# Kernel optimization log

Hardware: AMD Instinct MI355X
Metric: run time of the kernel (lower is better)

The kernel has to match this reference:

```python
import jax, jax.numpy as jnp
from jax import lax
import numpy as np

BATCH, SEQ_LEN, INPUT_DIM, HIDDEN, NUM_CLASSES = 2048, 512, 1, 1024, 10


def setup_inputs() -> dict:
    key = jax.random.key(0)
    k1, k2, k3, k4 = jax.random.split(key, 4)
    x = jax.random.normal(k1, (BATCH, SEQ_LEN), dtype=jnp.float32)
    # Parameters match torch.randn init; biases start at zero.
    W_hx = jax.random.normal(k2, (INPUT_DIM, HIDDEN), dtype=jnp.float32)
    W_hh = jax.random.normal(k3, (HIDDEN, HIDDEN), dtype=jnp.float32)
    W_ph = jax.random.normal(k4, (HIDDEN, NUM_CLASSES), dtype=jnp.float32)
    b_h = jnp.zeros((HIDDEN,), dtype=jnp.float32)
    b_p = jnp.zeros((NUM_CLASSES,), dtype=jnp.float32)
    return {"x": x, "W_hx": W_hx, "W_hh": W_hh, "W_ph": W_ph, "b_h": b_h, "b_p": b_p}


def reference(x, W_hx, W_hh, W_ph, b_h, b_p):
    # x: [B, T]; each timestep uses a single scalar feature -> [B, 1] @ [1, H]
    B = x.shape[0]
    H = W_hh.shape[0]

    def step(h, x_t):
        # x_t: [B]; h: [B, H]
        h_new = jnp.tanh(x_t[:, None] @ W_hx + h @ W_hh + b_h)
        return h_new, None

    h0 = jnp.zeros((B, H), dtype=x.dtype)
    h_T, _ = lax.scan(step, h0, x.T)  # scan over time (leading axis T)
    # Only the final timestep's projection is returned (matches original loop).
    return h_T @ W_ph + b_p  # [B, num_classes]
```

## Files before the change

### kernel.cpp

```cpp
#include <hip/hip_runtime.h>


#define SEQ   512
#define HID   1024
#define NCLS  10
#define TPB   512
#define ROWS  8
#define CLAMPV 7.99881172180175781f

__device__ __forceinline__ float tanh_win(float x) {
#pragma clang fp contract(off)
    float xc = fminf(fmaxf(x, -CLAMPV), CLAMPV);
    float x2 = xc * xc;
    float p = -2.76076847742355e-16f;
    p = __fmaf_rn(x2, p,  2.00018790482477e-13f);
    p = __fmaf_rn(x2, p, -8.60467152213735e-11f);
    p = __fmaf_rn(x2, p,  5.12229709037114e-08f);
    p = __fmaf_rn(x2, p,  1.48572235717979e-05f);
    p = __fmaf_rn(x2, p,  6.37261928875436e-04f);
    p = __fmaf_rn(x2, p,  4.89352455891786e-03f);
    p = xc * p;
    float q = 1.19825839466702e-06f;
    q = __fmaf_rn(x2, q,  1.18534705686654e-04f);
    q = __fmaf_rn(x2, q,  2.26843463243900e-03f);
    q = __fmaf_rn(x2, q,  4.89352518554385e-03f);
    float r = p / q;
    return (fabsf(x) < 0.0004f) ? x : r;
}

#define MAC4(hv, wv)                              \
    sv.x = __fmaf_rn((hv), (wv).x, sv.x);         \
    sv.y = __fmaf_rn((hv), (wv).y, sv.y);         \
    sv.z = __fmaf_rn((hv), (wv).z, sv.z);         \
    sv.w = __fmaf_rn((hv), (wv).w, sv.w);

__device__ __forceinline__ void panel512(float4 s[ROWS],
                                         const float* __restrict__ hl,
                                         const float* __restrict__ Whh,
                                         int ks, int c0) {
#pragma clang fp contract(off)
    #pragma unroll
    for (int r = 0; r < ROWS; ++r) s[r] = float4{0.f, 0.f, 0.f, 0.f};

    unsigned off = (unsigned)(ks * HID + c0);
    #pragma unroll 2
    for (int j = ks; j < ks + 512; j += 8) {
        const float4 w0 = *reinterpret_cast<const float4*>(Whh + off);
        const float4 w1 = *reinterpret_cast<const float4*>(Whh + off + 1u * HID);
        const float4 w2 = *reinterpret_cast<const float4*>(Whh + off + 2u * HID);
        const float4 w3 = *reinterpret_cast<const float4*>(Whh + off + 3u * HID);
        const float4 w4 = *reinterpret_cast<const float4*>(Whh + off + 4u * HID);
        const float4 w5 = *reinterpret_cast<const float4*>(Whh + off + 5u * HID);
        const float4 w6 = *reinterpret_cast<const float4*>(Whh + off + 6u * HID);
        const float4 w7 = *reinterpret_cast<const float4*>(Whh + off + 7u * HID);
        off += 8u * HID;
        #pragma unroll
        for (int r = 0; r < ROWS; ++r) {
            const float4 ha = *reinterpret_cast<const float4*>(&hl[r * HID + j]);
            const float4 hb = *reinterpret_cast<const float4*>(&hl[r * HID + j + 4]);
            float4 sv = s[r];
            MAC4(ha.x, w0); MAC4(ha.y, w1); MAC4(ha.z, w2); MAC4(ha.w, w3);
            MAC4(hb.x, w4); MAC4(hb.y, w5); MAC4(hb.z, w6); MAC4(hb.w, w7);
            s[r] = sv;
        }
    }
}

__launch_bounds__(TPB, 1)
__global__ void rnn_win(const float* __restrict__ x, const float* __restrict__ W_hx,
                        const float* __restrict__ Whh, const float* __restrict__ W_ph,
                        const float* __restrict__ bh, const float* __restrict__ bp,
                        float* __restrict__ out) {
#pragma clang fp contract(off)
    __shared__ float hl[ROWS * HID];
    __shared__ float xl[ROWS * SEQ];
    __shared__ float sb[ROWS * HID];
    const int tid  = threadIdx.x;
    const int blk  = blockIdx.x;
    const int lane = tid & 255;
    const int pp   = tid >> 8;
    const int c0   = lane * 4;
    const int row0 = blk * ROWS;

    for (int i = tid; i < ROWS * SEQ; i += TPB) xl[i] = x[(size_t)row0 * SEQ + i];
    for (int i = tid; i < ROWS * HID; i += TPB) hl[i] = 0.0f;

    const float4 w4 = *reinterpret_cast<const float4*>(W_hx + c0);
    const float4 b4 = *reinterpret_cast<const float4*>(bh + c0);
    __syncthreads();

    for (int t = 0; t < SEQ; ++t) {
        float4 s[ROWS];
        panel512(s, hl, Whh, pp * 512, c0);

        if (pp == 1) {
            #pragma unroll
            for (int r = 0; r < ROWS; ++r)
                *reinterpret_cast<float4*>(&sb[r * HID + c0]) = s[r];
        }
        __syncthreads();

        if (pp == 0) {
            #pragma unroll
            for (int r = 0; r < ROWS; ++r) {
                const float4 s1 = *reinterpret_cast<const float4*>(&sb[r * HID + c0]);
                const float xv = xl[r * SEQ + t];
                float4 g;
                g.x = s[r].x + s1.x;
                g.y = s[r].y + s1.y;
                g.z = s[r].z + s1.z;
                g.w = s[r].w + s1.w;
                float4 hn;
                hn.x = tanh_win(__fmaf_rn(xv, w4.x, g.x) + b4.x);
                hn.y = tanh_win(__fmaf_rn(xv, w4.y, g.y) + b4.y);
                hn.z = tanh_win(__fmaf_rn(xv, w4.z, g.z) + b4.z);
                hn.w = tanh_win(__fmaf_rn(xv, w4.w, g.w) + b4.w);
                *reinterpret_cast<float4*>(&hl[r * HID + c0]) = hn;
            }
        }
        __syncthreads();
    }

    if (tid < ROWS * NCLS) {
        const int r = tid / NCLS, k = tid - r * NCLS;
        float acc = bp[k];
        for (int j = 0; j < HID; ++j)
            acc = __fmaf_rn(hl[r * HID + j], W_ph[j * NCLS + k], acc);
        out[(size_t)(row0 + r) * NCLS + k] = acc;
    }
}

extern "C" void kernel_launch(void* const* d_in, const int* in_sizes, int n_in,
                              void* d_out, int out_size, void* d_ws, size_t ws_size,
                              hipStream_t stream) {
    const float* x    = (const float*)d_in[0];
    const float* W_hx = (const float*)d_in[1];
    const float* Whh  = (const float*)d_in[2];
    const float* W_ph = (const float*)d_in[3];
    const float* bh   = (const float*)d_in[4];
    const float* bp   = (const float*)d_in[5];
    float* out = (float*)d_out;

    rnn_win<<<2048 / ROWS, TPB, 0, stream>>>(x, W_hx, Whh, W_ph, bh, bp, out);
}
```

Before: 28.26 ms.

## Double-buffer W_hh register loads and split tanh epilogue across both halves

The W_hh panel loop becomes a two-stage register pipeline: the next 8-row weight group is loaded while FMAs run on the current group. The tanh/update epilogue is split so each 256-thread half finalizes 4 of the 8 rows, exchanging partial sums through shared memory, instead of one half doing all rows. Launch bounds now request 2 blocks per CU. Two risks come with this: the tighter register budget, and indexing the accumulator array by a runtime half index, could cause spills. With 256 blocks there is only one block per CU anyway, so the occupancy request does not help.

```diff
diff --git a/kernel.cpp b/kernel.cpp
--- a/kernel.cpp
+++ b/kernel.cpp
@@ -34,39 +34,33 @@
     sv.z = __fmaf_rn((hv), (wv).z, sv.z);         \
     sv.w = __fmaf_rn((hv), (wv).w, sv.w);
 
-__device__ __forceinline__ void panel512(float4 s[ROWS],
-                                         const float* __restrict__ hl,
-                                         const float* __restrict__ Whh,
-                                         int ks, int c0) {
+__device__ __forceinline__ void loadgrp(float4 w[8], const float* __restrict__ Whh,
+                                        unsigned off) {
+    w[0] = *reinterpret_cast<const float4*>(Whh + off);
+    w[1] = *reinterpret_cast<const float4*>(Whh + off + 1u * HID);
+    w[2] = *reinterpret_cast<const float4*>(Whh + off + 2u * HID);
+    w[3] = *reinterpret_cast<const float4*>(Whh + off + 3u * HID);
+    w[4] = *reinterpret_cast<const float4*>(Whh + off + 4u * HID);
+    w[5] = *reinterpret_cast<const float4*>(Whh + off + 5u * HID);
+    w[6] = *reinterpret_cast<const float4*>(Whh + off + 6u * HID);
+    w[7] = *reinterpret_cast<const float4*>(Whh + off + 7u * HID);
+}
+
+__device__ __forceinline__ void fmagrp(float4 s[ROWS], const float4 w[8],
+                                       const float* __restrict__ hl, int j) {
 #pragma clang fp contract(off)
     #pragma unroll
-    for (int r = 0; r < ROWS; ++r) s[r] = float4{0.f, 0.f, 0.f, 0.f};
-
-    unsigned off = (unsigned)(ks * HID + c0);
-    #pragma unroll 2
-    for (int j = ks; j < ks + 512; j += 8) {
-        const float4 w0 = *reinterpret_cast<const float4*>(Whh + off);
-        const float4 w1 = *reinterpret_cast<const float4*>(Whh + off + 1u * HID);
-        const float4 w2 = *reinterpret_cast<const float4*>(Whh + off + 2u * HID);
-        const float4 w3 = *reinterpret_cast<const float4*>(Whh + off + 3u * HID);
-        const float4 w4 = *reinterpret_cast<const float4*>(Whh + off + 4u * HID);
-        const float4 w5 = *reinterpret_cast<const float4*>(Whh + off + 5u * HID);
-        const float4 w6 = *reinterpret_cast<const float4*>(Whh + off + 6u * HID);
-        const float4 w7 = *reinterpret_cast<const float4*>(Whh + off + 7u * HID);
-        off += 8u * HID;
-        #pragma unroll
-        for (int r = 0; r < ROWS; ++r) {
-            const float4 ha = *reinterpret_cast<const float4*>(&hl[r * HID + j]);
-            const float4 hb = *reinterpret_cast<const float4*>(&hl[r * HID + j + 4]);
-            float4 sv = s[r];
-            MAC4(ha.x, w0); MAC4(ha.y, w1); MAC4(ha.z, w2); MAC4(ha.w, w3);
-            MAC4(hb.x, w4); MAC4(hb.y, w5); MAC4(hb.z, w6); MAC4(hb.w, w7);
-            s[r] = sv;
-        }
+    for (int r = 0; r < ROWS; ++r) {
+        const float4 ha = *reinterpret_cast<const float4*>(&hl[r * HID + j]);
+        const float4 hb = *reinterpret_cast<const float4*>(&hl[r * HID + j + 4]);
+        float4 sv = s[r];
+        MAC4(ha.x, w[0]); MAC4(ha.y, w[1]); MAC4(ha.z, w[2]); MAC4(ha.w, w[3]);
+        MAC4(hb.x, w[4]); MAC4(hb.y, w[5]); MAC4(hb.z, w[6]); MAC4(hb.w, w[7]);
+        s[r] = sv;
     }
 }
 
-__launch_bounds__(TPB, 1)
+__launch_bounds__(TPB, 2)
 __global__ void rnn_win(const float* __restrict__ x, const float* __restrict__ W_hx,
                         const float* __restrict__ Whh, const float* __restrict__ W_ph,
                         const float* __restrict__ bh, const float* __restrict__ bp,
@@ -77,9 +71,9 @@
     __shared__ float sb[ROWS * HID];
     const int tid  = threadIdx.x;
     const int blk  = blockIdx.x;
-    const int lane = tid & 255;
+    const int col  = tid & 255;
     const int pp   = tid >> 8;
-    const int c0   = lane * 4;
+    const int c0   = col * 4;
     const int row0 = blk * ROWS;
 
     for (int i = tid; i < ROWS * SEQ; i += TPB) xl[i] = x[(size_t)row0 * SEQ + i];
@@ -87,36 +81,55 @@
 
     const float4 w4 = *reinterpret_cast<const float4*>(W_hx + c0);
     const float4 b4 = *reinterpret_cast<const float4*>(bh + c0);
+    const unsigned off0 = (unsigned)(pp * 512 * HID + c0);
+    const int frbase = pp * 4;
+    const int prbase = 4 - frbase;
     __syncthreads();
 
     for (int t = 0; t < SEQ; ++t) {
         float4 s[ROWS];
-        panel512(s, hl, Whh, pp * 512, c0);
+        #pragma unroll
+        for (int r = 0; r < ROWS; ++r) s[r] = float4{0.f, 0.f, 0.f, 0.f};
 
-        if (pp == 1) {
-            #pragma unroll
-            for (int r = 0; r < ROWS; ++r)
-                *reinterpret_cast<float4*>(&sb[r * HID + c0]) = s[r];
+        {
+            float4 wA[8], wB[8];
+            unsigned off = off0;
+            const int jb = pp * 512;
+            loadgrp(wA, Whh, off);
+            #pragma unroll 1
+            for (int g = 0; g < 62; g += 2) {
+                loadgrp(wB, Whh, off + 8u * HID);
+                fmagrp(s, wA, hl, jb + g * 8);
+                loadgrp(wA, Whh, off + 16u * HID);
+                fmagrp(s, wB, hl, jb + g * 8 + 8);
+                off += 16u * HID;
+            }
+            loadgrp(wB, Whh, off + 8u * HID);
+            fmagrp(s, wA, hl, jb + 62 * 8);
+            fmagrp(s, wB, hl, jb + 63 * 8);
         }
+
+        #pragma unroll
+        for (int r = 0; r < 4; ++r)
+            *reinterpret_cast<float4*>(&sb[(prbase + r) * HID + c0]) = s[prbase + r];
         __syncthreads();
 
-        if (pp == 0) {
-            #pragma unroll
-            for (int r = 0; r < ROWS; ++r) {
-                const float4 s1 = *reinterpret_cast<const float4*>(&sb[r * HID + c0]);
-                const float xv = xl[r * SEQ + t];
-                float4 g;
-                g.x = s[r].x + s1.x;
-                g.y = s[r].y + s1.y;
-                g.z = s[r].z + s1.z;
-                g.w = s[r].w + s1.w;
-                float4 hn;
-                hn.x = tanh_win(__fmaf_rn(xv, w4.x, g.x) + b4.x);
-                hn.y = tanh_win(__fmaf_rn(xv, w4.y, g.y) + b4.y);
-                hn.z = tanh_win(__fmaf_rn(xv, w4.z, g.z) + b4.z);
-                hn.w = tanh_win(__fmaf_rn(xv, w4.w, g.w) + b4.w);
-                *reinterpret_cast<float4*>(&hl[r * HID + c0]) = hn;
-            }
+        #pragma unroll
+        for (int r = 0; r < 4; ++r) {
+            const int row = frbase + r;
+            const float4 so = *reinterpret_cast<const float4*>(&sb[row * HID + c0]);
+            const float xv = xl[row * SEQ + t];
+            float4 g;
+            g.x = s[row].x + so.x;
+            g.y = s[row].y + so.y;
+            g.z = s[row].z + so.z;
+            g.w = s[row].w + so.w;
+            float4 hn;
+            hn.x = tanh_win(__fmaf_rn(xv, w4.x, g.x) + b4.x);
+            hn.y = tanh_win(__fmaf_rn(xv, w4.y, g.y) + b4.y);
+            hn.z = tanh_win(__fmaf_rn(xv, w4.z, g.z) + b4.z);
+            hn.w = tanh_win(__fmaf_rn(xv, w4.w, g.w) + b4.w);
+            *reinterpret_cast<float4*>(&hl[row * HID + c0]) = hn;
         }
         __syncthreads();
     }
```

New measurement: 31.79 ms. 1.12x slower.
